# Optimization experiments

Measured on AMD Instinct MI355X. Metric: run time of the kernel, lower is better.

The kernel has to match this reference:

```python
import jax, jax.numpy as jnp
import numpy as np

SQRT_DK = np.sqrt(512.0).astype(np.float32)


def setup_inputs() -> dict:
    key = jax.random.key(0)
    k1, k2, k3 = jax.random.split(key, 3)
    x = jax.random.normal(k1, (16, 2048, 512), dtype=jnp.float32)
    W1 = jax.random.normal(k2, (512, 10), dtype=jnp.float32) * 0.05
    W2 = jax.random.normal(k3, (10, 512), dtype=jnp.float32) * 0.05
    return {"x": x, "W1": W1, "W2": W2}


def reference(x, W1, W2):
    # x: [B, A, D]; low-rank bilinear scores: (x@W1) @ (W2@x^T) -> [B, A, A]
    B, A, D = x.shape
    left = jnp.einsum('bad,dr->bar', x, W1)          # [B, A, 10]
    right = jnp.einsum('rd,bcd->brc', W2, x)         # [B, 10, A]
    scores = jnp.einsum('bar,brc->bac', left, right)  # [B, A, A]
    attn = jax.nn.softmax(scores / SQRT_DK, axis=-1)
    out = jnp.einsum('bac,bcd->bad', attn, x)         # requires_value=True
    return out
```

## Files before the change

### kernel.cpp

```cpp
#include <hip/hip_runtime.h>
#include <cstdint>
#include <cstddef>


typedef float    f32x4 __attribute__((ext_vector_type(4)));
typedef _Float16 half8 __attribute__((ext_vector_type(8)));
typedef _Float16 half4 __attribute__((ext_vector_type(4)));

#define B_  16
#define A_  2048
#define D_  512
#define KSCALE 0.06375872f

#define SCHED_FENCE() __builtin_amdgcn_sched_barrier(0)

__device__ inline float fast_exp2(float v) {
#if __has_builtin(__builtin_amdgcn_exp2f)
    return __builtin_amdgcn_exp2f(v);
#else
    return __expf(v * 0.6931471805599453f);
#endif
}

__global__ __launch_bounds__(256) void kw_prep(const float* __restrict__ W1,
                                               const float* __restrict__ W2,
                                               _Float16* __restrict__ Wf) {
    int pi = blockIdx.x * 256 + threadIdx.x;
    int kt = pi >> 6, lane = pi & 63;
    int quad = lane >> 4, col = lane & 15;
    half8 h1, h2;
#pragma unroll
    for (int j = 0; j < 8; ++j) {
        int d = kt * 32 + quad * 8 + j;
        h1[j] = (col < 10) ? (_Float16)(W1[d * 10 + col] * KSCALE) : (_Float16)0.f;
        h2[j] = (col < 10) ? (_Float16)W2[col * 512 + d] : (_Float16)0.f;
    }
    *(half8*)(Wf + (size_t)pi * 16) = h1;
    *(half8*)(Wf + (size_t)pi * 16 + 8) = h2;
}

__global__ __launch_bounds__(256) void kt_transpose(const float* __restrict__ x,
                                                    _Float16* __restrict__ xT) {
    __shared__ float xs[128 * 64];
    int t = threadIdx.x, w = t >> 6;
    int bid = blockIdx.x;
    int b = bid >> 7, cg = (bid >> 3) & 15, dg = bid & 7;
    int c0 = cg << 7, d0 = dg << 6;
    const float* xb = x + ((size_t)(b * A_ + c0)) * D_ + d0;
#pragma unroll
    for (int it = 0; it < 8; ++it) {
        int slot = it * 256 + t;
        int c = slot >> 4, g = slot & 15;
        int gs = g ^ (c >> 3);
        const float* src = xb + (size_t)c * D_ + (gs << 2);
        float* dst = xs + (size_t)(it * 256 + w * 64) * 4;
        __builtin_amdgcn_global_load_lds((const __attribute__((address_space(1))) void*)src,
                                         (__attribute__((address_space(3))) void*)dst,
                                         16, 0, 0);
    }
    __syncthreads();
    _Float16* xTb = xT + ((size_t)b * D_ + d0) * A_ + c0;
#pragma unroll
    for (int p = 0; p < 4; ++p) {
        int dloc = p * 16 + (t >> 4);
        int c8 = (t & 15) << 3;
        int gd = dloc >> 2, e = dloc & 3;
        half8 h;
#pragma unroll
        for (int j = 0; j < 8; ++j) {
            int c = c8 + j;
            h[j] = (_Float16)xs[c * 64 + ((gd ^ (c >> 3)) << 2) + e];
        }
        *(half8*)(xTb + (size_t)dloc * A_ + c8) = h;
    }
}

__global__ __launch_bounds__(256) void kf_factors(const float* __restrict__ x,
                                                  const _Float16* __restrict__ Wf,
                                                  _Float16* __restrict__ left16,
                                                  _Float16* __restrict__ rightT16) {
    int t = threadIdx.x, lane = t & 63, w = t >> 6;
    int quad = lane >> 4, c16 = lane & 15;
    size_t arow0 = (size_t)blockIdx.x * 64 + (size_t)w * 16;
    const float* xa = x + (arow0 + c16) * D_;
    f32x4 accA = {0.f, 0.f, 0.f, 0.f}, accB = {0.f, 0.f, 0.f, 0.f};
#pragma unroll
    for (int kc = 0; kc < 16; ++kc) {
        float4 v0 = *(const float4*)(xa + kc * 32 + quad * 8);
        float4 v1 = *(const float4*)(xa + kc * 32 + quad * 8 + 4);
        half8 af;
        af[0] = (_Float16)v0.x; af[1] = (_Float16)v0.y; af[2] = (_Float16)v0.z; af[3] = (_Float16)v0.w;
        af[4] = (_Float16)v1.x; af[5] = (_Float16)v1.y; af[6] = (_Float16)v1.z; af[7] = (_Float16)v1.w;
        const half8* wf = (const half8*)(Wf + ((size_t)(kc * 64 + lane)) * 16);
        accA = __builtin_amdgcn_mfma_f32_16x16x32_f16(af, wf[0], accA, 0, 0, 0);
        accB = __builtin_amdgcn_mfma_f32_16x16x32_f16(af, wf[1], accB, 0, 0, 0);
    }
#pragma unroll
    for (int q = 0; q < 4; ++q) {
        size_t grow = arow0 + (size_t)quad * 4 + q;
        left16[grow * 16 + c16]   = (_Float16)accA[q];
        rightT16[grow * 16 + c16] = (_Float16)accB[q];
    }
}

__global__ __launch_bounds__(512, 4) void k3_attn(const _Float16* __restrict__ xT,
                                                  const _Float16* __restrict__ left16,
                                                  const _Float16* __restrict__ rightT16,
                                                  float* __restrict__ out) {
    __shared__ _Float16 XTl[2][256 * 32];
    __shared__ _Float16 Ps[2][128 * 40];
    __shared__ float rowsum[128];
    int t = threadIdx.x, lane = t & 63, w = t >> 6;
    int quad = lane >> 4, c16 = lane & 15;
    int bid = blockIdx.x;
    int combo = (bid & 7) | (((bid >> 7) & 3) << 3);
    int at = (bid >> 3) & 15;
    int b = combo >> 1, nb = combo & 1;
    int a0 = at << 7, n0 = nb << 8;
    int waveM = w & 1, waveN = w >> 1;

    half8 lf8 = (half8)(_Float16)0.f;
    if (quad < 2) {
        int arow = a0 + w * 16 + c16;
        lf8 = *(const half8*)(left16 + ((size_t)(b << 11) + arow) * 16 + quad * 8);
    }

    f32x4 acc[4][4];
#pragma unroll
    for (int mi = 0; mi < 4; ++mi)
#pragma unroll
        for (int ni = 0; ni < 4; ++ni) acc[mi][ni] = (f32x4){0.f, 0.f, 0.f, 0.f};
    float psum = 0.f;

    const _Float16* xTb = xT + ((size_t)b * D_ + n0) * A_;
    const _Float16* rTb = rightT16 + (size_t)(b << 11) * 16;

    int nloc0 = w * 32 + (lane >> 2);
    int kq = lane & 3;
    int psrow = (w * 16 + c16) * 40;

    auto dma_tile = [&](int kt, int buf) {
        int c0 = kt << 5;
#pragma unroll
        for (int cc = 0; cc < 2; ++cc) {
            int nl = nloc0 + cc * 16;
            int kqs = kq ^ ((nl >> 1) & 3);
            const _Float16* src = xTb + (size_t)nl * A_ + c0 + kqs * 8;
            _Float16* dst = &XTl[buf][(w * 32 + cc * 16) * 32];
            __builtin_amdgcn_global_load_lds((const __attribute__((address_space(1))) void*)src,
                                             (__attribute__((address_space(3))) void*)dst,
                                             16, 0, 0);
        }
    };
    auto load_bfr = [&](int kt, half8* bfr) {
#pragma unroll
        for (int nh = 0; nh < 2; ++nh) {
            bfr[nh] = (half8)(_Float16)0.f;
            if (quad < 2) {
                int crow = (kt << 5) + nh * 16 + c16;
                bfr[nh] = *(const half8*)(rTb + (size_t)crow * 16 + quad * 8);
            }
        }
    };

    half8 bfr_cur[2], bfr_nxt[2];
    load_bfr(0, bfr_cur);
    dma_tile(0, 0);
    {
        f32x4 zz = {0.f, 0.f, 0.f, 0.f};
        f32x4 p0 = __builtin_amdgcn_mfma_f32_16x16x32_f16(bfr_cur[0], lf8, zz, 0, 0, 0);
        f32x4 p1 = __builtin_amdgcn_mfma_f32_16x16x32_f16(bfr_cur[1], lf8, zz, 0, 0, 0);
        float e0 = fast_exp2(p0[0]), e1 = fast_exp2(p0[1]), e2 = fast_exp2(p0[2]), e3 = fast_exp2(p0[3]);
        float f0 = fast_exp2(p1[0]), f1 = fast_exp2(p1[1]), f2 = fast_exp2(p1[2]), f3 = fast_exp2(p1[3]);
        psum += (e0 + e1) + (e2 + e3) + (f0 + f1) + (f2 + f3);
        half4 pv0, pv1;
        pv0[0] = (_Float16)e0; pv0[1] = (_Float16)e1; pv0[2] = (_Float16)e2; pv0[3] = (_Float16)e3;
        pv1[0] = (_Float16)f0; pv1[1] = (_Float16)f1; pv1[2] = (_Float16)f2; pv1[3] = (_Float16)f3;
        *(half4*)&Ps[0][psrow + quad * 4] = pv0;
        *(half4*)&Ps[0][psrow + 16 + quad * 4] = pv1;
    }
    load_bfr(1, bfr_cur);

    for (int kt = 0; kt < 63; ++kt) {
        __syncthreads();
        int cb = kt & 1, nx = kt + 1;

        f32x4 zz = {0.f, 0.f, 0.f, 0.f};
        f32x4 pc0 = __builtin_amdgcn_mfma_f32_16x16x32_f16(bfr_cur[0], lf8, zz, 0, 0, 0);
        f32x4 pc1 = __builtin_amdgcn_mfma_f32_16x16x32_f16(bfr_cur[1], lf8, zz, 0, 0, 0);
        dma_tile(nx, nx & 1);
        {
            int ktn = (kt + 2 < 64) ? kt + 2 : 0;
            load_bfr(ktn, bfr_nxt);
        }
        half8 bf[4];
#pragma unroll
        for (int ni = 0; ni < 4; ++ni) {
            int nr = waveN * 64 + ni * 16 + c16;
            bf[ni] = *(const half8*)&XTl[cb][nr * 32 + ((quad ^ ((nr >> 1) & 3)) << 3)];
        }
        half8 af0 = *(const half8*)&Ps[cb][(waveM * 64 + c16) * 40 + quad * 8];
        SCHED_FENCE();

        half8 af1 = *(const half8*)&Ps[cb][(waveM * 64 + 16 + c16) * 40 + quad * 8];
#pragma unroll
        for (int ni = 0; ni < 4; ++ni)
            acc[0][ni] = __builtin_amdgcn_mfma_f32_16x16x32_f16(af0, bf[ni], acc[0][ni], 0, 0, 0);
        float e0 = fast_exp2(pc0[0]), e1 = fast_exp2(pc0[1]);
        float e2 = fast_exp2(pc0[2]), e3 = fast_exp2(pc0[3]);
        psum += (e0 + e1) + (e2 + e3);
        half4 pv0;
        pv0[0] = (_Float16)e0; pv0[1] = (_Float16)e1; pv0[2] = (_Float16)e2; pv0[3] = (_Float16)e3;
        SCHED_FENCE();

        half8 af2 = *(const half8*)&Ps[cb][(waveM * 64 + 32 + c16) * 40 + quad * 8];
#pragma unroll
        for (int ni = 0; ni < 4; ++ni)
            acc[1][ni] = __builtin_amdgcn_mfma_f32_16x16x32_f16(af1, bf[ni], acc[1][ni], 0, 0, 0);
        float f0 = fast_exp2(pc1[0]), f1 = fast_exp2(pc1[1]);
        float f2 = fast_exp2(pc1[2]), f3 = fast_exp2(pc1[3]);
        psum += (f0 + f1) + (f2 + f3);
        half4 pv1;
        pv1[0] = (_Float16)f0; pv1[1] = (_Float16)f1; pv1[2] = (_Float16)f2; pv1[3] = (_Float16)f3;
        SCHED_FENCE();

        half8 af3 = *(const half8*)&Ps[cb][(waveM * 64 + 48 + c16) * 40 + quad * 8];
#pragma unroll
        for (int ni = 0; ni < 4; ++ni)
            acc[2][ni] = __builtin_amdgcn_mfma_f32_16x16x32_f16(af2, bf[ni], acc[2][ni], 0, 0, 0);
        *(half4*)&Ps[nx & 1][psrow + quad * 4] = pv0;
        SCHED_FENCE();

#pragma unroll
        for (int ni = 0; ni < 4; ++ni)
            acc[3][ni] = __builtin_amdgcn_mfma_f32_16x16x32_f16(af3, bf[ni], acc[3][ni], 0, 0, 0);
        *(half4*)&Ps[nx & 1][psrow + 16 + quad * 4] = pv1;
        bfr_cur[0] = bfr_nxt[0];
        bfr_cur[1] = bfr_nxt[1];
    }

    __syncthreads();
    {
        const int cb = 1;
        half8 bf[4];
#pragma unroll
        for (int ni = 0; ni < 4; ++ni) {
            int nr = waveN * 64 + ni * 16 + c16;
            bf[ni] = *(const half8*)&XTl[cb][nr * 32 + ((quad ^ ((nr >> 1) & 3)) << 3)];
        }
#pragma unroll
        for (int mi = 0; mi < 4; ++mi) {
            half8 af = *(const half8*)&Ps[cb][(waveM * 64 + mi * 16 + c16) * 40 + quad * 8];
#pragma unroll
            for (int ni = 0; ni < 4; ++ni)
                acc[mi][ni] = __builtin_amdgcn_mfma_f32_16x16x32_f16(af, bf[ni], acc[mi][ni], 0, 0, 0);
        }
    }

    {
        float s = psum;
        s += __shfl_xor(s, 16);
        s += __shfl_xor(s, 32);
        if (quad == 0) rowsum[w * 16 + c16] = s;
    }
    __syncthreads();

    float* ob = out + ((size_t)b * A_ + a0) * D_ + n0;
#pragma unroll
    for (int mi = 0; mi < 4; ++mi) {
#pragma unroll
        for (int q = 0; q < 4; ++q) {
            int ar = waveM * 64 + mi * 16 + quad * 4 + q;
            float sc = 1.0f / rowsum[ar];
#pragma unroll
            for (int ni = 0; ni < 4; ++ni)
                ob[(size_t)ar * D_ + waveN * 64 + ni * 16 + c16] = acc[mi][ni][q] * sc;
        }
    }
}

extern "C" void kernel_launch(void* const* d_in, const int* in_sizes, int n_in,
                              void* d_out, int out_size, void* d_ws, size_t ws_size,
                              hipStream_t stream) {
    const float* x  = (const float*)d_in[0];
    const float* W1 = (const float*)d_in[1];
    const float* W2 = (const float*)d_in[2];
    float* out = (float*)d_out;
    char* ws = (char*)d_ws;
    _Float16* xT      = (_Float16*)ws;
    _Float16* left16  = (_Float16*)(ws + 33554432);
    _Float16* rightT16= (_Float16*)(ws + 34603008);
    _Float16* Wf      = (_Float16*)(ws + 35651584);

    kw_prep<<<4, 256, 0, stream>>>(W1, W2, Wf);
    kt_transpose<<<2048, 256, 0, stream>>>(x, xT);
    kf_factors<<<512, 256, 0, stream>>>(x, Wf, left16, rightT16);
    k3_attn<<<512, 512, 0, stream>>>(xT, left16, rightT16, out);
}
```

Baseline: 203.7 us.

## Retile attention block to 64 query rows by full 512-wide D

Each block now covers 64 query rows and the whole 512-column value width, where it used to cover 128 rows and half of D. Every wave handles a 64-column slice of D for all 64 rows. The score/exp work for the 64x32 P tile is split across the two wave halves, and their partial row sums are combined through shared memory. This removes the duplicated score and exp computation across the two D halves, but doubles the xT tile staged per block and increases LDS use per block, which may lower occupancy.

```diff
diff --git a/kernel.cpp b/kernel.cpp
--- a/kernel.cpp
+++ b/kernel.cpp
@@ -107,21 +107,20 @@
                                                   const _Float16* __restrict__ left16,
                                                   const _Float16* __restrict__ rightT16,
                                                   float* __restrict__ out) {
-    __shared__ _Float16 XTl[2][256 * 32];
-    __shared__ _Float16 Ps[2][128 * 40];
-    __shared__ float rowsum[128];
+    __shared__ _Float16 XTl[2][512 * 32];
+    __shared__ _Float16 Ps[2][64 * 40];
+    __shared__ float red[2][64];
     int t = threadIdx.x, lane = t & 63, w = t >> 6;
     int quad = lane >> 4, c16 = lane & 15;
     int bid = blockIdx.x;
-    int combo = (bid & 7) | (((bid >> 7) & 3) << 3);
-    int at = (bid >> 3) & 15;
-    int b = combo >> 1, nb = combo & 1;
-    int a0 = at << 7, n0 = nb << 8;
-    int waveM = w & 1, waveN = w >> 1;
+    int b = (bid & 7) | (((bid >> 8) & 1) << 3);
+    int at = (bid >> 3) & 31;
+    int a0 = at << 6;
+    int agrp = w & 3, chalf = w >> 2;
 
     half8 lf8 = (half8)(_Float16)0.f;
     if (quad < 2) {
-        int arow = a0 + w * 16 + c16;
+        int arow = a0 + agrp * 16 + c16;
         lf8 = *(const half8*)(left16 + ((size_t)(b << 11) + arow) * 16 + quad * 8);
     }
 
@@ -132,111 +131,99 @@
         for (int ni = 0; ni < 4; ++ni) acc[mi][ni] = (f32x4){0.f, 0.f, 0.f, 0.f};
     float psum = 0.f;
 
-    const _Float16* xTb = xT + ((size_t)b * D_ + n0) * A_;
+    const _Float16* xTb = xT + (size_t)b * D_ * A_;
     const _Float16* rTb = rightT16 + (size_t)(b << 11) * 16;
 
-    int nloc0 = w * 32 + (lane >> 2);
+    int nloc0 = w * 64 + (lane >> 2);
     int kq = lane & 3;
-    int psrow = (w * 16 + c16) * 40;
+    int psrow = (agrp * 16 + c16) * 40 + chalf * 16;
 
     auto dma_tile = [&](int kt, int buf) {
         int c0 = kt << 5;
 #pragma unroll
-        for (int cc = 0; cc < 2; ++cc) {
+        for (int cc = 0; cc < 4; ++cc) {
             int nl = nloc0 + cc * 16;
             int kqs = kq ^ ((nl >> 1) & 3);
             const _Float16* src = xTb + (size_t)nl * A_ + c0 + kqs * 8;
-            _Float16* dst = &XTl[buf][(w * 32 + cc * 16) * 32];
+            _Float16* dst = &XTl[buf][(w * 64 + cc * 16) * 32];
             __builtin_amdgcn_global_load_lds((const __attribute__((address_space(1))) void*)src,
                                              (__attribute__((address_space(3))) void*)dst,
                                              16, 0, 0);
         }
     };
-    auto load_bfr = [&](int kt, half8* bfr) {
-#pragma unroll
-        for (int nh = 0; nh < 2; ++nh) {
-            bfr[nh] = (half8)(_Float16)0.f;
-            if (quad < 2) {
-                int crow = (kt << 5) + nh * 16 + c16;
-                bfr[nh] = *(const half8*)(rTb + (size_t)crow * 16 + quad * 8);
-            }
-        }
+    auto load_bfr = [&](int kt) {
+        half8 bfr = (half8)(_Float16)0.f;
+        if (quad < 2) {
+            int crow = (kt << 5) + chalf * 16 + c16;
+            bfr = *(const half8*)(rTb + (size_t)crow * 16 + quad * 8);
+        }
+        return bfr;
     };
 
-    half8 bfr_cur[2], bfr_nxt[2];
-    load_bfr(0, bfr_cur);
+    half8 bfr_cur, bfr_nxt;
+    bfr_cur = load_bfr(0);
     dma_tile(0, 0);
     {
         f32x4 zz = {0.f, 0.f, 0.f, 0.f};
-        f32x4 p0 = __builtin_amdgcn_mfma_f32_16x16x32_f16(bfr_cur[0], lf8, zz, 0, 0, 0);
-        f32x4 p1 = __builtin_amdgcn_mfma_f32_16x16x32_f16(bfr_cur[1], lf8, zz, 0, 0, 0);
-        float e0 = fast_exp2(p0[0]), e1 = fast_exp2(p0[1]), e2 = fast_exp2(p0[2]), e3 = fast_exp2(p0[3]);
-        float f0 = fast_exp2(p1[0]), f1 = fast_exp2(p1[1]), f2 = fast_exp2(p1[2]), f3 = fast_exp2(p1[3]);
-        psum += (e0 + e1) + (e2 + e3) + (f0 + f1) + (f2 + f3);
-        half4 pv0, pv1;
-        pv0[0] = (_Float16)e0; pv0[1] = (_Float16)e1; pv0[2] = (_Float16)e2; pv0[3] = (_Float16)e3;
-        pv1[0] = (_Float16)f0; pv1[1] = (_Float16)f1; pv1[2] = (_Float16)f2; pv1[3] = (_Float16)f3;
-        *(half4*)&Ps[0][psrow + quad * 4] = pv0;
-        *(half4*)&Ps[0][psrow + 16 + quad * 4] = pv1;
-    }
-    load_bfr(1, bfr_cur);
+        f32x4 p0 = __builtin_amdgcn_mfma_f32_16x16x32_f16(bfr_cur, lf8, zz, 0, 0, 0);
+        float e0 = fast_exp2(p0[0]), e1 = fast_exp2(p0[1]);
+        float e2 = fast_exp2(p0[2]), e3 = fast_exp2(p0[3]);
+        psum += (e0 + e1) + (e2 + e3);
+        half4 pv;
+        pv[0] = (_Float16)e0; pv[1] = (_Float16)e1; pv[2] = (_Float16)e2; pv[3] = (_Float16)e3;
+        *(half4*)&Ps[0][psrow + quad * 4] = pv;
+    }
+    bfr_cur = load_bfr(1);
 
     for (int kt = 0; kt < 63; ++kt) {
         __syncthreads();
         int cb = kt & 1, nx = kt + 1;
 
         f32x4 zz = {0.f, 0.f, 0.f, 0.f};
-        f32x4 pc0 = __builtin_amdgcn_mfma_f32_16x16x32_f16(bfr_cur[0], lf8, zz, 0, 0, 0);
-        f32x4 pc1 = __builtin_amdgcn_mfma_f32_16x16x32_f16(bfr_cur[1], lf8, zz, 0, 0, 0);
+        f32x4 pc0 = __builtin_amdgcn_mfma_f32_16x16x32_f16(bfr_cur, lf8, zz, 0, 0, 0);
         dma_tile(nx, nx & 1);
         {
             int ktn = (kt + 2 < 64) ? kt + 2 : 0;
-            load_bfr(ktn, bfr_nxt);
+            bfr_nxt = load_bfr(ktn);
         }
         half8 bf[4];
 #pragma unroll
         for (int ni = 0; ni < 4; ++ni) {
-            int nr = waveN * 64 + ni * 16 + c16;
+            int nr = w * 64 + ni * 16 + c16;
             bf[ni] = *(const half8*)&XTl[cb][nr * 32 + ((quad ^ ((nr >> 1) & 3)) << 3)];
         }
-        half8 af0 = *(const half8*)&Ps[cb][(waveM * 64 + c16) * 40 + quad * 8];
-        SCHED_FENCE();
-
-        half8 af1 = *(const half8*)&Ps[cb][(waveM * 64 + 16 + c16) * 40 + quad * 8];
+        half8 af0 = *(const half8*)&Ps[cb][(c16) * 40 + quad * 8];
+        SCHED_FENCE();
+
+        half8 af1 = *(const half8*)&Ps[cb][(16 + c16) * 40 + quad * 8];
 #pragma unroll
         for (int ni = 0; ni < 4; ++ni)
             acc[0][ni] = __builtin_amdgcn_mfma_f32_16x16x32_f16(af0, bf[ni], acc[0][ni], 0, 0, 0);
         float e0 = fast_exp2(pc0[0]), e1 = fast_exp2(pc0[1]);
+        psum += (e0 + e1);
+        SCHED_FENCE();
+
+        half8 af2 = *(const half8*)&Ps[cb][(32 + c16) * 40 + quad * 8];
+#pragma unroll
+        for (int ni = 0; ni < 4; ++ni)
+            acc[1][ni] = __builtin_amdgcn_mfma_f32_16x16x32_f16(af1, bf[ni], acc[1][ni], 0, 0, 0);
         float e2 = fast_exp2(pc0[2]), e3 = fast_exp2(pc0[3]);
-        psum += (e0 + e1) + (e2 + e3);
-        half4 pv0;
-        pv0[0] = (_Float16)e0; pv0[1] = (_Float16)e1; pv0[2] = (_Float16)e2; pv0[3] = (_Float16)e3;
-        SCHED_FENCE();
-
-        half8 af2 = *(const half8*)&Ps[cb][(waveM * 64 + 32 + c16) * 40 + quad * 8];
-#pragma unroll
-        for (int ni = 0; ni < 4; ++ni)
-            acc[1][ni] = __builtin_amdgcn_mfma_f32_16x16x32_f16(af1, bf[ni], acc[1][ni], 0, 0, 0);
-        float f0 = fast_exp2(pc1[0]), f1 = fast_exp2(pc1[1]);
-        float f2 = fast_exp2(pc1[2]), f3 = fast_exp2(pc1[3]);
-        psum += (f0 + f1) + (f2 + f3);
-        half4 pv1;
-        pv1[0] = (_Float16)f0; pv1[1] = (_Float16)f1; pv1[2] = (_Float16)f2; pv1[3] = (_Float16)f3;
-        SCHED_FENCE();
-
-        half8 af3 = *(const half8*)&Ps[cb][(waveM * 64 + 48 + c16) * 40 + quad * 8];
+        psum += (e2 + e3);
+        half4 pv;
+        pv[0] = (_Float16)e0; pv[1] = (_Float16)e1; pv[2] = (_Float16)e2; pv[3] = (_Float16)e3;
+        SCHED_FENCE();
+
+        half8 af3 = *(const half8*)&Ps[cb][(48 + c16) * 40 + quad * 8];
 #pragma unroll
         for (int ni = 0; ni < 4; ++ni)
             acc[2][ni] = __builtin_amdgcn_mfma_f32_16x16x32_f16(af2, bf[ni], acc[2][ni], 0, 0, 0);
-        *(half4*)&Ps[nx & 1][psrow + quad * 4] = pv0;
+        *(half4*)&Ps[nx & 1][psrow + quad * 4] = pv;
         SCHED_FENCE();
 
 #pragma unroll
         for (int ni = 0; ni < 4; ++ni)
             acc[3][ni] = __builtin_amdgcn_mfma_f32_16x16x32_f16(af3, bf[ni], acc[3][ni], 0, 0, 0);
-        *(half4*)&Ps[nx & 1][psrow + 16 + quad * 4] = pv1;
-        bfr_cur[0] = bfr_nxt[0];
-        bfr_cur[1] = bfr_nxt[1];
+        bfr_cur = bfr_nxt;
     }
 
     __syncthreads();
@@ -245,12 +232,12 @@
         half8 bf[4];
 #pragma unroll
         for (int ni = 0; ni < 4; ++ni) {
-            int nr = waveN * 64 + ni * 16 + c16;
+            int nr = w * 64 + ni * 16 + c16;
             bf[ni] = *(const half8*)&XTl[cb][nr * 32 + ((quad ^ ((nr >> 1) & 3)) << 3)];
         }
 #pragma unroll
         for (int mi = 0; mi < 4; ++mi) {
-            half8 af = *(const half8*)&Ps[cb][(waveM * 64 + mi * 16 + c16) * 40 + quad * 8];
+            half8 af = *(const half8*)&Ps[cb][(mi * 16 + c16) * 40 + quad * 8];
 #pragma unroll
             for (int ni = 0; ni < 4; ++ni)
                 acc[mi][ni] = __builtin_amdgcn_mfma_f32_16x16x32_f16(af, bf[ni], acc[mi][ni], 0, 0, 0);
@@ -261,20 +248,20 @@
         float s = psum;
         s += __shfl_xor(s, 16);
         s += __shfl_xor(s, 32);
-        if (quad == 0) rowsum[w * 16 + c16] = s;
+        if (quad == 0 && agrp == (int)(w & 3)) red[chalf][agrp * 16 + c16] = s;
     }
     __syncthreads();
 
-    float* ob = out + ((size_t)b * A_ + a0) * D_ + n0;
+    float* ob = out + ((size_t)b * A_ + a0) * D_;
 #pragma unroll
     for (int mi = 0; mi < 4; ++mi) {
 #pragma unroll
         for (int q = 0; q < 4; ++q) {
-            int ar = waveM * 64 + mi * 16 + quad * 4 + q;
-            float sc = 1.0f / rowsum[ar];
+            int ar = mi * 16 + quad * 4 + q;
+            float sc = 1.0f / (red[0][ar] + red[1][ar]);
 #pragma unroll
             for (int ni = 0; ni < 4; ++ni)
-                ob[(size_t)ar * D_ + waveN * 64 + ni * 16 + c16] = acc[mi][ni][q] * sc;
+                ob[(size_t)ar * D_ + w * 64 + ni * 16 + c16] = acc[mi][ni][q] * sc;
         }
     }
 }
```

Result: slower. 211.4 us (+3.8%).

## Fuse transpose and low-rank factor kernels into one pass over x

Applied to the files above, without the earlier changes.

Merges the fp16 transpose kernel and the factor-projection kernel into a single kernel, so x is read from global memory once instead of twice. Each block stages 32 rows by 64 columns of x in swizzled LDS, writes the transposed fp16 tile, and feeds MFMA for the left/right factors with a split-K across wave pairs followed by an LDS reduction. This saves one 64MB read and one launch, but adds per-chunk barriers and a smaller, less latency-hiding tile pipeline without async global-to-LDS loads.

```diff
diff --git a/kernel.cpp b/kernel.cpp
--- a/kernel.cpp
+++ b/kernel.cpp
@@ -6,6 +6,7 @@
 typedef float    f32x4 __attribute__((ext_vector_type(4)));
 typedef _Float16 half8 __attribute__((ext_vector_type(8)));
 typedef _Float16 half4 __attribute__((ext_vector_type(4)));
+typedef _Float16 half2 __attribute__((ext_vector_type(2)));
 
 #define B_  16
 #define A_  2048
@@ -39,67 +40,75 @@
     *(half8*)(Wf + (size_t)pi * 16 + 8) = h2;
 }
 
-__global__ __launch_bounds__(256) void kt_transpose(const float* __restrict__ x,
-                                                    _Float16* __restrict__ xT) {
-    __shared__ float xs[128 * 64];
-    int t = threadIdx.x, w = t >> 6;
-    int bid = blockIdx.x;
-    int b = bid >> 7, cg = (bid >> 3) & 15, dg = bid & 7;
-    int c0 = cg << 7, d0 = dg << 6;
-    const float* xb = x + ((size_t)(b * A_ + c0)) * D_ + d0;
-#pragma unroll
-    for (int it = 0; it < 8; ++it) {
-        int slot = it * 256 + t;
-        int c = slot >> 4, g = slot & 15;
-        int gs = g ^ (c >> 3);
-        const float* src = xb + (size_t)c * D_ + (gs << 2);
-        float* dst = xs + (size_t)(it * 256 + w * 64) * 4;
-        __builtin_amdgcn_global_load_lds((const __attribute__((address_space(1))) void*)src,
-                                         (__attribute__((address_space(3))) void*)dst,
-                                         16, 0, 0);
-    }
-    __syncthreads();
-    _Float16* xTb = xT + ((size_t)b * D_ + d0) * A_ + c0;
-#pragma unroll
-    for (int p = 0; p < 4; ++p) {
-        int dloc = p * 16 + (t >> 4);
-        int c8 = (t & 15) << 3;
-        int gd = dloc >> 2, e = dloc & 3;
-        half8 h;
-#pragma unroll
-        for (int j = 0; j < 8; ++j) {
-            int c = c8 + j;
-            h[j] = (_Float16)xs[c * 64 + ((gd ^ (c >> 3)) << 2) + e];
-        }
-        *(half8*)(xTb + (size_t)dloc * A_ + c8) = h;
-    }
-}
-
-__global__ __launch_bounds__(256) void kf_factors(const float* __restrict__ x,
-                                                  const _Float16* __restrict__ Wf,
-                                                  _Float16* __restrict__ left16,
-                                                  _Float16* __restrict__ rightT16) {
+__global__ __launch_bounds__(256) void k01_prep(const float* __restrict__ x,
+                                                const _Float16* __restrict__ Wf,
+                                                _Float16* __restrict__ xT,
+                                                _Float16* __restrict__ left16,
+                                                _Float16* __restrict__ rightT16) {
+    __shared__ float xs[32 * 64];
     int t = threadIdx.x, lane = t & 63, w = t >> 6;
     int quad = lane >> 4, c16 = lane & 15;
-    size_t arow0 = (size_t)blockIdx.x * 64 + (size_t)w * 16;
-    const float* xa = x + (arow0 + c16) * D_;
+    int bid = blockIdx.x;
+    int b = bid >> 6, grp = bid & 63;
+    int c0 = grp << 5;
+    const float* xb = x + ((size_t)b * A_ + c0) * D_;
+    int tile = w >> 1, kki = w & 1;
+    int ar = tile * 16 + c16;
     f32x4 accA = {0.f, 0.f, 0.f, 0.f}, accB = {0.f, 0.f, 0.f, 0.f};
-#pragma unroll
-    for (int kc = 0; kc < 16; ++kc) {
-        float4 v0 = *(const float4*)(xa + kc * 32 + quad * 8);
-        float4 v1 = *(const float4*)(xa + kc * 32 + quad * 8 + 4);
-        half8 af;
-        af[0] = (_Float16)v0.x; af[1] = (_Float16)v0.y; af[2] = (_Float16)v0.z; af[3] = (_Float16)v0.w;
-        af[4] = (_Float16)v1.x; af[5] = (_Float16)v1.y; af[6] = (_Float16)v1.z; af[7] = (_Float16)v1.w;
-        const half8* wf = (const half8*)(Wf + ((size_t)(kc * 64 + lane)) * 16);
-        accA = __builtin_amdgcn_mfma_f32_16x16x32_f16(af, wf[0], accA, 0, 0, 0);
-        accB = __builtin_amdgcn_mfma_f32_16x16x32_f16(af, wf[1], accB, 0, 0, 0);
-    }
-#pragma unroll
-    for (int q = 0; q < 4; ++q) {
-        size_t grow = arow0 + (size_t)quad * 4 + q;
-        left16[grow * 16 + c16]   = (_Float16)accA[q];
-        rightT16[grow * 16 + c16] = (_Float16)accB[q];
+
+    for (int dc = 0; dc < 8; ++dc) {
+        __syncthreads();
+#pragma unroll
+        for (int p = 0; p < 2; ++p) {
+            int c = p * 16 + (t >> 4), ch = t & 15;
+            float4 v = *(const float4*)(xb + (size_t)c * D_ + dc * 64 + ch * 4);
+            *(float4*)&xs[c * 64 + ((ch ^ (c & 15)) << 2)] = v;
+        }
+        __syncthreads();
+        {
+            int dloc = t >> 2, c8 = (t & 3) << 3;
+            int ch = dloc >> 2, e = dloc & 3;
+            half8 h;
+#pragma unroll
+            for (int j = 0; j < 8; ++j) {
+                int c = c8 + j;
+                h[j] = (_Float16)xs[c * 64 + ((ch ^ (c & 15)) << 2) + e];
+            }
+            *(half8*)(xT + ((size_t)b * D_ + dc * 64 + dloc) * A_ + c0 + c8) = h;
+        }
+        {
+            int kk = kki * 32;
+            int ch0 = (kk >> 2) + quad * 2;
+            float4 v0 = *(const float4*)&xs[ar * 64 + ((ch0 ^ c16) << 2)];
+            float4 v1 = *(const float4*)&xs[ar * 64 + (((ch0 + 1) ^ c16) << 2)];
+            half8 af;
+            af[0] = (_Float16)v0.x; af[1] = (_Float16)v0.y; af[2] = (_Float16)v0.z; af[3] = (_Float16)v0.w;
+            af[4] = (_Float16)v1.x; af[5] = (_Float16)v1.y; af[6] = (_Float16)v1.z; af[7] = (_Float16)v1.w;
+            const half8* wf = (const half8*)(Wf + ((size_t)((dc * 2 + kki) * 64 + lane)) * 16);
+            half8 b1 = wf[0], b2 = wf[1];
+            accA = __builtin_amdgcn_mfma_f32_16x16x32_f16(af, b1, accA, 0, 0, 0);
+            accB = __builtin_amdgcn_mfma_f32_16x16x32_f16(af, b2, accB, 0, 0, 0);
+        }
+    }
+    __syncthreads();
+    float* red = xs;
+    if (kki == 0) {
+#pragma unroll
+        for (int q = 0; q < 4; ++q) {
+            red[tile * 512 + (quad * 4 + q) * 16 + c16] = accA[q];
+            red[tile * 512 + 256 + (quad * 4 + q) * 16 + c16] = accB[q];
+        }
+    }
+    __syncthreads();
+    if (kki == 1) {
+#pragma unroll
+        for (int q = 0; q < 4; ++q) {
+            float a = accA[q] + red[tile * 512 + (quad * 4 + q) * 16 + c16];
+            float bb = accB[q] + red[tile * 512 + 256 + (quad * 4 + q) * 16 + c16];
+            size_t grow = (size_t)bid * 32 + tile * 16 + quad * 4 + q;
+            left16[grow * 16 + c16] = (_Float16)a;
+            rightT16[grow * 16 + c16] = (_Float16)bb;
+        }
     }
 }
 
@@ -293,7 +302,6 @@
     _Float16* Wf      = (_Float16*)(ws + 35651584);
 
     kw_prep<<<4, 256, 0, stream>>>(W1, W2, Wf);
-    kt_transpose<<<2048, 256, 0, stream>>>(x, xT);
-    kf_factors<<<512, 256, 0, stream>>>(x, Wf, left16, rightT16);
+    k01_prep<<<1024, 256, 0, stream>>>(x, Wf, xT, left16, rightT16);
     k3_attn<<<512, 512, 0, stream>>>(xT, left16, rightT16, out);
 }
```

Result: no change. 206.3 us (+1.3%).
